# Kernel tuning notes

Measured on AMD Instinct MI355X. Metric: run time of the kernel, lower is better.

Reference implementation:

```python
import jax, jax.numpy as jnp
import numpy as np

DIM = 384
NUM_HEADS = 12
HEAD_DIM = DIM // NUM_HEADS  # 32
SCALE = HEAD_DIM ** -0.5
B, N = 4, 2048


def setup_inputs() -> dict:
    key = jax.random.key(0)
    k0, k1, k2, k3 = jax.random.split(key, 4)
    x = jax.random.normal(k0, (B, N, DIM), dtype=jnp.float32)
    # nn.Linear(dim, 3*dim, bias=False): y = x @ W_qkv, W_qkv is [C, 3C]
    W_qkv = jax.random.normal(k1, (DIM, 3 * DIM), dtype=jnp.float32) * (DIM ** -0.5)
    # nn.Linear(dim, dim): y = x @ W_proj + b_proj, W_proj is [C, C]
    W_proj = jax.random.normal(k2, (DIM, DIM), dtype=jnp.float32) * (DIM ** -0.5)
    b_proj = jax.random.normal(k3, (DIM,), dtype=jnp.float32) * 0.01
    return {"x": x, "W_qkv": W_qkv, "W_proj": W_proj, "b_proj": b_proj}


def reference(x, W_qkv, W_proj, b_proj):
    b, n, c = x.shape
    qkv = (x @ W_qkv).reshape(b, n, 3, NUM_HEADS, HEAD_DIM)
    qkv = jnp.transpose(qkv, (2, 0, 3, 1, 4))  # [3, B, H, N, hd]
    q, k, v = qkv[0], qkv[1], qkv[2]
    # full attention: softmax(q k^T * scale) v
    attn = jnp.einsum('bhqd,bhkd->bhqk', q, k) * SCALE  # [B,H,N,N]
    attn = jax.nn.softmax(attn, axis=-1)
    out = jnp.einsum('bhqk,bhkd->bhqd', attn, v)  # [B,H,N,hd]
    out = jnp.transpose(out, (0, 2, 1, 3)).reshape(b, n, c)
    return out @ W_proj + b_proj
```

## Files before the change

kernel.cpp:

```cpp
#include <hip/hip_runtime.h>

constexpr int BB  = 4;
constexpr int SEQ = 2048;
constexpr int CC  = 384;
constexpr int C3  = 1152;
constexpr int NH  = 12;
constexpr int HD  = 32;
constexpr float SCALE = 0.17677669529663689f;
constexpr float LOG2E = 1.4426950408889634f;
constexpr float KSC   = SCALE * LOG2E;
constexpr size_t KV_BYTES = (size_t)2 * BB * NH * SEQ * HD * 2;
constexpr size_t WT_BYTES = ((size_t)C3 * CC + (size_t)CC * CC) * 2;
constexpr size_t XB_BYTES = (size_t)BB * SEQ * CC * 2;

typedef __attribute__((ext_vector_type(8))) short short8_t;
typedef __attribute__((ext_vector_type(4))) float floatx4;

#if __has_builtin(__builtin_amdgcn_exp2f)
#define EXP2F __builtin_amdgcn_exp2f
#else
#define EXP2F __builtin_exp2f
#endif

__device__ __forceinline__ unsigned short f2bf(float f) {
    unsigned int u = __builtin_bit_cast(unsigned int, f);
    u += 0x7fffu + ((u >> 16) & 1u);
    return (unsigned short)(u >> 16);
}
__device__ __forceinline__ unsigned int pk_rn(float lo, float hi) {
    return __builtin_amdgcn_perm(__builtin_bit_cast(unsigned int, hi) + 0x8000u,
                                 __builtin_bit_cast(unsigned int, lo) + 0x8000u,
                                 0x07060302u);
}
__device__ __forceinline__ unsigned int cvtpk(float lo, float hi) {
    unsigned int r;
    asm("v_cvt_pk_bf16_f32 %0, %1, %2" : "=v"(r) : "v"(lo), "v"(hi));
    return r;
}
__device__ __forceinline__ short8_t pack8(float4 a, float4 b) {
    uint4 u;
    u.x = pk_rn(a.x, a.y); u.y = pk_rn(a.z, a.w);
    u.z = pk_rn(b.x, b.y); u.w = pk_rn(b.z, b.w);
    return __builtin_bit_cast(short8_t, u);
}

__device__ __forceinline__ void vstore(unsigned short* vb, short8_t a, short8_t b) {
    const uint4 ua = __builtin_bit_cast(uint4, a);
    const uint4 ub = __builtin_bit_cast(uint4, b);
    *(uint2*)(vb)      = (uint2){ua.x, ua.y};
    *(uint2*)(vb + 8)  = (uint2){ua.z, ua.w};
    *(uint2*)(vb + 16) = (uint2){ub.x, ub.y};
    *(uint2*)(vb + 24) = (uint2){ub.z, ub.w};
}

__global__ __launch_bounds__(256) void prep_kernel(
    const float* __restrict__ x, const float* __restrict__ wqkv,
    const float* __restrict__ wproj,
    unsigned short* __restrict__ wqkvT, unsigned short* __restrict__ wprojT,
    unsigned short* __restrict__ xb)
{
    const int bid = blockIdx.x;
    if (bid >= 144) {
        const size_t base = (size_t)(bid - 144) * 2048 + threadIdx.x * 8;
        const float4 a = *(const float4*)(x + base);
        const float4 b = *(const float4*)(x + base + 4);
        uint4 u;
        u.x = pk_rn(a.x, a.y); u.y = pk_rn(a.z, a.w);
        u.z = pk_rn(b.x, b.y); u.w = pk_rn(b.z, b.w);
        *(uint4*)(xb + base) = u;
        return;
    }
    __shared__ float ls[64][68];
    const float* src; unsigned short* dst; int SN, k0, n0;
    if (bid < 108) {
        src = wqkv; dst = wqkvT; SN = C3;
        k0 = (bid / 18) * 64; n0 = (bid % 18) * 64;
    } else {
        const int b2 = bid - 108;
        src = wproj; dst = wprojT; SN = CC;
        k0 = (b2 / 6) * 64; n0 = (b2 % 6) * 64;
    }
    const int t  = threadIdx.x;
    const int rr = t >> 4, cc4 = (t & 15) * 4;
#pragma unroll
    for (int p = 0; p < 4; ++p) {
        const int row = p * 16 + rr;
        const float4 v = *(const float4*)&src[(size_t)(k0 + row) * SN + n0 + cc4];
        ls[row][cc4] = v.x; ls[row][cc4 + 1] = v.y;
        ls[row][cc4 + 2] = v.z; ls[row][cc4 + 3] = v.w;
    }
    __syncthreads();
#pragma unroll
    for (int p = 0; p < 4; ++p) {
        const int nrow = p * 16 + rr;
        uint2 u;
        u.x = pk_rn(ls[cc4][nrow],     ls[cc4 + 1][nrow]);
        u.y = pk_rn(ls[cc4 + 2][nrow], ls[cc4 + 3][nrow]);
        *(uint2*)&dst[(size_t)(n0 + nrow) * CC + k0 + cc4] = u;
    }
}

__global__ __launch_bounds__(256) void qkv_fast(
    const unsigned short* __restrict__ xb,
    const unsigned short* __restrict__ wT,
    unsigned short* __restrict__ qb,
    unsigned short* __restrict__ kv)
{
    __shared__ __align__(16) unsigned short As[2][128][40];
    __shared__ __align__(16) unsigned short Bs[2][128][40];

    const int mt   = blockIdx.x & 63;
    const int nb   = blockIdx.x >> 6;
    const int tid  = threadIdx.x;
    const int wid  = tid >> 6;
    const int lane = tid & 63;
    const int quad = lane >> 4;
    const int col  = lane & 15;
    const int wr   = wid >> 1, wc = wid & 1;
    const int m0 = mt * 128, n0 = nb * 128;

    const int arow = tid >> 1;
    const int aoff = (tid & 1) * 16;

    floatx4 acc[4][4];
#pragma unroll
    for (int i = 0; i < 4; ++i)
#pragma unroll
        for (int j = 0; j < 4; ++j) acc[i][j] = (floatx4){0.f, 0.f, 0.f, 0.f};

    const unsigned short* xrow = xb + (size_t)(m0 + arow) * CC + aoff;
    const unsigned short* wrow = wT + (size_t)(n0 + arow) * CC + aoff;

    short8_t ast0, ast1, bst0, bst1;
    ast0 = *(const short8_t*)xrow;
    ast1 = *(const short8_t*)(xrow + 8);
    bst0 = *(const short8_t*)wrow;
    bst1 = *(const short8_t*)(wrow + 8);
    *(short8_t*)&As[0][arow][aoff]     = ast0;
    *(short8_t*)&As[0][arow][aoff + 8] = ast1;
    *(short8_t*)&Bs[0][arow][aoff]     = bst0;
    *(short8_t*)&Bs[0][arow][aoff + 8] = bst1;

    for (int it = 0; it < CC / 32; ++it) {
        const int kn = (it + 1 < CC / 32) ? (it + 1) * 32 : 0;
        ast0 = *(const short8_t*)(xrow + kn);
        ast1 = *(const short8_t*)(xrow + kn + 8);
        bst0 = *(const short8_t*)(wrow + kn);
        bst1 = *(const short8_t*)(wrow + kn + 8);

        __syncthreads();
        const int p = it & 1;
        short8_t af[4], bf[4];
#pragma unroll
        for (int i = 0; i < 4; ++i)
            af[i] = *(const short8_t*)&As[p][wr * 64 + i * 16 + col][quad * 8];
#pragma unroll
        for (int j = 0; j < 4; ++j)
            bf[j] = *(const short8_t*)&Bs[p][wc * 64 + j * 16 + col][quad * 8];
#pragma unroll
        for (int j = 0; j < 4; ++j)
#pragma unroll
            for (int i = 0; i < 4; ++i)
                acc[i][j] = __builtin_amdgcn_mfma_f32_16x16x32_bf16(af[i], bf[j], acc[i][j], 0, 0, 0);

        *(short8_t*)&As[p ^ 1][arow][aoff]     = ast0;
        *(short8_t*)&As[p ^ 1][arow][aoff + 8] = ast1;
        *(short8_t*)&Bs[p ^ 1][arow][aoff]     = bst0;
        *(short8_t*)&Bs[p ^ 1][arow][aoff + 8] = bst1;
    }

    const int t = nb / 3;
#pragma unroll
    for (int i = 0; i < 4; ++i) {
        const int mg = m0 + wr * 64 + i * 16 + quad * 4;
        if (t == 0) {
#pragma unroll
            for (int j = 0; j < 4; ++j) {
                const int n = n0 + wc * 64 + j * 16 + col;
#pragma unroll
                for (int r = 0; r < 4; ++r)
                    qb[(size_t)(mg + r) * CC + n] = f2bf(acc[i][j][r]);
            }
        } else if (t == 1) {
            const int b = mg >> 11, s = mg & (SEQ - 1);
#pragma unroll
            for (int j = 0; j < 4; ++j) {
                const int rem = n0 - CC + wc * 64 + j * 16 + col;
                const int h = rem >> 5, d = rem & 31;
                unsigned short* kp = kv + ((size_t)(b * NH + h) * SEQ + s) * HD + d;
#pragma unroll
                for (int r = 0; r < 4; ++r)
                    kp[(size_t)r * HD] = f2bf(acc[i][j][r] * KSC);
            }
        } else {
            const int b = mg >> 11, s = mg & (SEQ - 1);
            unsigned short* vtb = kv + (size_t)BB * NH * SEQ * HD;
#pragma unroll
            for (int j = 0; j < 4; ++j) {
                const int rem = n0 - 2 * CC + wc * 64 + j * 16 + col;
                const int h = rem >> 5, d = rem & 31;
                uint2 u;
                u.x = pk_rn(acc[i][j][0], acc[i][j][1]);
                u.y = pk_rn(acc[i][j][2], acc[i][j][3]);
                *(uint2*)&vtb[((size_t)(b * NH + h) * HD + d) * SEQ + s] = u;
            }
        }
    }
}

__global__ __launch_bounds__(256, 3) void attn_kernel(
    const unsigned short* __restrict__ kv,
    const unsigned short* __restrict__ qb,
    unsigned short* __restrict__ ab)
{
    const int bid  = blockIdx.x;
    const int qp   = bid / 48;
    const int bh   = bid % 48;
    const int h    = bh % NH;
    const int b    = bh / NH;
    const int w    = threadIdx.x >> 6;
    const int lane = threadIdx.x & 63;
    const int quad = lane >> 4;
    const int col  = lane & 15;
    const int tid  = threadIdx.x;

    const unsigned short* K  = kv + (size_t)bh * SEQ * HD;
    const unsigned short* VT = kv + (size_t)BB * NH * SEQ * HD + (size_t)bh * HD * SEQ;

    __shared__ __align__(16) unsigned short Vt[2][32][136];

    const int drow_s = tid >> 3, voff_s = (tid & 7) * 16;
    const int vbase  = ((tid & 6) >> 1) * 32 + (tid & 1) * 4;

    const unsigned short* Kf = K + (size_t)col * HD + quad * 8;

    int qrow[2];
    short8_t qf[2];
#pragma unroll
    for (int t = 0; t < 2; ++t) {
        qrow[t] = b * SEQ + qp * 128 + (w + 4 * t) * 16 + col;
        qf[t] = *(const short8_t*)(qb + (size_t)qrow[t] * CC + h * HD + quad * 8);
    }

    short8_t ones;
#pragma unroll
    for (int e = 0; e < 8; ++e) ones[e] = (short)0x3F80;

    floatx4 o[2][2];
    floatx4 lacc[2];
#pragma unroll
    for (int t = 0; t < 2; ++t) {
        lacc[t] = (floatx4){0.f, 0.f, 0.f, 0.f};
#pragma unroll
        for (int i = 0; i < 2; ++i) o[t][i] = (floatx4){0.f, 0.f, 0.f, 0.f};
    }
    const float ci = -10.f * LOG2E;
    const floatx4 cinit = {ci, ci, ci, ci};

    short8_t v0a = *(const short8_t*)(VT + (size_t)drow_s * SEQ + voff_s);
    short8_t v0b = *(const short8_t*)(VT + (size_t)drow_s * SEQ + voff_s + 8);
    vstore(&Vt[0][drow_s][vbase], v0a, v0b);

    short8_t kaf[4][2];
#pragma unroll
    for (int c = 0; c < 4; ++c) {
        kaf[c][0] = *(const short8_t*)(Kf + (size_t)(c * 32) * HD);
        kaf[c][1] = *(const short8_t*)(Kf + (size_t)(c * 32 + 16) * HD);
    }

    for (int it = 0; it < SEQ / 128; ++it) {
        const int kn = ((it + 1) * 128) & (SEQ - 1);
        v0a = *(const short8_t*)(VT + (size_t)drow_s * SEQ + kn + voff_s);
        v0b = *(const short8_t*)(VT + (size_t)drow_s * SEQ + kn + voff_s + 8);
        const unsigned short* Kn = Kf + (size_t)kn * HD;

        __syncthreads();
        const int p = it & 1;

        short8_t va[4][2];
#pragma unroll
        for (int c = 0; c < 4; ++c) {
            const int c32 = c * 32;
            va[c][0] = *(const short8_t*)&Vt[p][col][c32 + quad * 8];
            va[c][1] = *(const short8_t*)&Vt[p][16 + col][c32 + quad * 8];
        }

        floatx4 s0[2], s1[2];
        __builtin_amdgcn_s_setprio(1);
#pragma unroll
        for (int t = 0; t < 2; ++t) {
            s0[t] = __builtin_amdgcn_mfma_f32_16x16x32_bf16(kaf[0][0], qf[t], cinit, 0, 0, 0);
            s1[t] = __builtin_amdgcn_mfma_f32_16x16x32_bf16(kaf[0][1], qf[t], cinit, 0, 0, 0);
        }
        __builtin_amdgcn_s_setprio(0);
        kaf[0][0] = *(const short8_t*)(Kn);
        kaf[0][1] = *(const short8_t*)(Kn + (size_t)16 * HD);

#pragma unroll
        for (int c = 0; c < 4; ++c) {
            floatx4 n0[2], n1[2];
            if (c < 3) {
                __builtin_amdgcn_s_setprio(1);
#pragma unroll
                for (int t = 0; t < 2; ++t) {
                    n0[t] = __builtin_amdgcn_mfma_f32_16x16x32_bf16(kaf[c + 1][0], qf[t], cinit, 0, 0, 0);
                    n1[t] = __builtin_amdgcn_mfma_f32_16x16x32_bf16(kaf[c + 1][1], qf[t], cinit, 0, 0, 0);
                }
                __builtin_amdgcn_s_setprio(0);
                kaf[c + 1][0] = *(const short8_t*)(Kn + (size_t)((c + 1) * 32) * HD);
                kaf[c + 1][1] = *(const short8_t*)(Kn + (size_t)((c + 1) * 32 + 16) * HD);
            }

            short8_t pb[2];
#pragma unroll
            for (int t = 0; t < 2; ++t) {
                const float p00 = EXP2F(s0[t][0]), p01 = EXP2F(s0[t][1]);
                const float p02 = EXP2F(s0[t][2]), p03 = EXP2F(s0[t][3]);
                const float p10 = EXP2F(s1[t][0]), p11 = EXP2F(s1[t][1]);
                const float p12 = EXP2F(s1[t][2]), p13 = EXP2F(s1[t][3]);
                const uint4 pu = {cvtpk(p00, p01), cvtpk(p02, p03),
                                  cvtpk(p10, p11), cvtpk(p12, p13)};
                pb[t] = __builtin_bit_cast(short8_t, pu);
            }
            __builtin_amdgcn_s_setprio(1);
#pragma unroll
            for (int t = 0; t < 2; ++t) {
                o[t][0] = __builtin_amdgcn_mfma_f32_16x16x32_bf16(va[c][0], pb[t], o[t][0], 0, 0, 0);
                o[t][1] = __builtin_amdgcn_mfma_f32_16x16x32_bf16(va[c][1], pb[t], o[t][1], 0, 0, 0);
                lacc[t] = __builtin_amdgcn_mfma_f32_16x16x32_bf16(ones, pb[t], lacc[t], 0, 0, 0);
            }
            __builtin_amdgcn_s_setprio(0);
            if (c < 3) {
#pragma unroll
                for (int t = 0; t < 2; ++t) { s0[t] = n0[t]; s1[t] = n1[t]; }
            }
        }

        vstore(&Vt[p ^ 1][drow_s][vbase], v0a, v0b);
    }

#pragma unroll
    for (int t = 0; t < 2; ++t) {
        const float inv = 1.f / lacc[t][0];
        unsigned short* op = ab + (size_t)qrow[t] * CC + h * HD;
#pragma unroll
        for (int i = 0; i < 2; ++i) {
            uint2 u;
            u.x = pk_rn(o[t][i][0] * inv, o[t][i][1] * inv);
            u.y = pk_rn(o[t][i][2] * inv, o[t][i][3] * inv);
            *(uint2*)&op[i * 16 + quad * 4] = u;
        }
    }
}

__global__ __launch_bounds__(512) void proj_fast(
    const unsigned short* __restrict__ ab,
    const unsigned short* __restrict__ wT,
    const float* __restrict__ bias,
    float* __restrict__ out)
{
    __shared__ __align__(16) unsigned short Bs[2][384][32];

    const int mt   = blockIdx.x;
    const int tid  = threadIdx.x;
    const int wid  = tid >> 6;
    const int wn   = wid & 3;
    const int wm   = wid >> 2;
    const int lane = tid & 63;
    const int quad = lane >> 4;
    const int col  = lane & 15;
    const int m0   = mt * 32;

    floatx4 acc[6];
#pragma unroll
    for (int j = 0; j < 6; ++j) acc[j] = (floatx4){0.f, 0.f, 0.f, 0.f};

    const unsigned short* arow = ab + (size_t)(m0 + wm * 16 + col) * CC + quad * 8;

    const int f1 = tid;
    const int f2 = 512 + tid;
    const bool has2 = tid < 256;
    const unsigned short* wp1 = wT + (size_t)(f1 >> 1) * CC + (f1 & 1) * 16;
    const unsigned short* wp2 = wT + (size_t)(f2 >> 1) * CC + (f2 & 1) * 16;

    short8_t bA0, bA1, bB0, bB1;
    short8_t af;
    {
        bA0 = *(const short8_t*)wp1;
        bA1 = *(const short8_t*)(wp1 + 8);
        if (has2) {
            bB0 = *(const short8_t*)wp2;
            bB1 = *(const short8_t*)(wp2 + 8);
        }
        af = *(const short8_t*)arow;
        *(short8_t*)&Bs[0][f1 >> 1][(f1 & 1) * 16]     = bA0;
        *(short8_t*)&Bs[0][f1 >> 1][(f1 & 1) * 16 + 8] = bA1;
        if (has2) {
            *(short8_t*)&Bs[0][f2 >> 1][(f2 & 1) * 16]     = bB0;
            *(short8_t*)&Bs[0][f2 >> 1][(f2 & 1) * 16 + 8] = bB1;
        }
    }

    for (int it = 0; it < CC / 32; ++it) {
        const int kn = (it + 1 < CC / 32) ? (it + 1) * 32 : 0;
        bA0 = *(const short8_t*)(wp1 + kn);
        bA1 = *(const short8_t*)(wp1 + kn + 8);
        if (has2) {
            bB0 = *(const short8_t*)(wp2 + kn);
            bB1 = *(const short8_t*)(wp2 + kn + 8);
        }
        const short8_t afn = *(const short8_t*)(arow + kn);

        __syncthreads();
        const int p = it & 1;
        short8_t bf[6];
#pragma unroll
        for (int j = 0; j < 6; ++j)
            bf[j] = *(const short8_t*)&Bs[p][wn * 96 + j * 16 + col][quad * 8];
#pragma unroll
        for (int j = 0; j < 6; ++j)
            acc[j] = __builtin_amdgcn_mfma_f32_16x16x32_bf16(af, bf[j], acc[j], 0, 0, 0);

        *(short8_t*)&Bs[p ^ 1][f1 >> 1][(f1 & 1) * 16]     = bA0;
        *(short8_t*)&Bs[p ^ 1][f1 >> 1][(f1 & 1) * 16 + 8] = bA1;
        if (has2) {
            *(short8_t*)&Bs[p ^ 1][f2 >> 1][(f2 & 1) * 16]     = bB0;
            *(short8_t*)&Bs[p ^ 1][f2 >> 1][(f2 & 1) * 16 + 8] = bB1;
        }
        af = afn;
    }

#pragma unroll
    for (int j = 0; j < 6; ++j) {
        const int n = wn * 96 + j * 16 + col;
        const float bv = bias[n];
#pragma unroll
        for (int r = 0; r < 4; ++r)
            out[(size_t)(m0 + wm * 16 + quad * 4 + r) * CC + n] = acc[j][r] + bv;
    }
}

__global__ __launch_bounds__(256) void qkv_lds(
    const float* __restrict__ x, const float* __restrict__ w,
    float* __restrict__ dq, unsigned short* __restrict__ kv)
{
    __shared__ __align__(16) unsigned short wt[128 * 40];
    const int mt = blockIdx.x & 63, nb = blockIdx.x >> 6;
    const int tid = threadIdx.x, wid = tid >> 6, lane = tid & 63;
    const int quad = lane >> 4, col = lane & 15;
    const int wr = wid >> 1, wc = wid & 1;
    const int m0 = mt * 128, n0 = nb * 128;
    const int sn = tid >> 1, skg = (tid & 1) * 4;

    floatx4 acc[4][4];
#pragma unroll
    for (int i = 0; i < 4; ++i)
#pragma unroll
        for (int j = 0; j < 4; ++j) acc[i][j] = (floatx4){0.f, 0.f, 0.f, 0.f};
    const float* xbase = x + (size_t)(m0 + wr * 64 + col) * CC;

    for (int kb = 0; kb < CC; kb += 32) {
        float wv[4][4];
#pragma unroll
        for (int s = 0; s < 4; ++s) {
            const int k = kb + (skg + s) * 4;
#pragma unroll
            for (int j = 0; j < 4; ++j) wv[s][j] = w[(size_t)(k + j) * C3 + n0 + sn];
        }
        short8_t af[4];
#pragma unroll
        for (int i = 0; i < 4; ++i) {
            const float* xr = xbase + (size_t)i * 16 * CC + kb + quad * 8;
            af[i] = pack8(*(const float4*)xr, *(const float4*)(xr + 4));
        }
        __syncthreads();
#pragma unroll
        for (int s = 0; s < 4; ++s) {
            ushort4 u;
            u.x = f2bf(wv[s][0]); u.y = f2bf(wv[s][1]);
            u.z = f2bf(wv[s][2]); u.w = f2bf(wv[s][3]);
            *(ushort4*)&wt[sn * 40 + (skg + s) * 4] = u;
        }
        __syncthreads();
#pragma unroll
        for (int j = 0; j < 4; ++j) {
            const short8_t bf = *(const short8_t*)&wt[(wc * 64 + j * 16 + col) * 40 + quad * 8];
#pragma unroll
            for (int i = 0; i < 4; ++i)
                acc[i][j] = __builtin_amdgcn_mfma_f32_16x16x32_bf16(af[i], bf, acc[i][j], 0, 0, 0);
        }
    }
    const int t = nb / 3;
#pragma unroll
    for (int i = 0; i < 4; ++i) {
        const int mg = m0 + wr * 64 + i * 16 + quad * 4;
        if (t == 0) {
#pragma unroll
            for (int j = 0; j < 4; ++j) {
                const int n = n0 + wc * 64 + j * 16 + col;
#pragma unroll
                for (int r = 0; r < 4; ++r) dq[(size_t)(mg + r) * CC + n] = acc[i][j][r];
            }
        } else if (t == 1) {
            const int b = mg >> 11, s = mg & (SEQ - 1);
#pragma unroll
            for (int j = 0; j < 4; ++j) {
                const int rem = n0 - CC + wc * 64 + j * 16 + col;
                const int h = rem >> 5, d = rem & 31;
                unsigned short* kp = kv + ((size_t)(b * NH + h) * SEQ + s) * HD + d;
#pragma unroll
                for (int r = 0; r < 4; ++r) kp[(size_t)r * HD] = f2bf(acc[i][j][r]);
            }
        } else {
            const int b = mg >> 11, s = mg & (SEQ - 1);
            unsigned short* vtb = kv + (size_t)BB * NH * SEQ * HD;
#pragma unroll
            for (int j = 0; j < 4; ++j) {
                const int rem = n0 - 2 * CC + wc * 64 + j * 16 + col;
                const int h = rem >> 5, d = rem & 31;
                uint2 u;
                u.x = pk_rn(acc[i][j][0], acc[i][j][1]);
                u.y = pk_rn(acc[i][j][2], acc[i][j][3]);
                *(uint2*)&vtb[((size_t)(b * NH + h) * HD + d) * SEQ + s] = u;
            }
        }
    }
}

__global__ __launch_bounds__(256) void attn_f32(
    const unsigned short* __restrict__ kv,
    float* qatt)
{
    const int bid  = blockIdx.x;
    const int qp   = bid / 48;
    const int bh   = bid % 48;
    const int h    = bh % NH;
    const int b    = bh / NH;
    const int w    = threadIdx.x >> 6;
    const int lane = threadIdx.x & 63;
    const int quad = lane >> 4;
    const int col  = lane & 15;
    const int tid  = threadIdx.x;

    const unsigned short* K  = kv + (size_t)bh * SEQ * HD;
    const unsigned short* VT = kv + (size_t)BB * NH * SEQ * HD + (size_t)bh * HD * SEQ;

    __shared__ __align__(16) unsigned short Kt[2][128][40];
    __shared__ __align__(16) unsigned short Vt[2][32][136];

    const int krow_s = tid >> 1, koff_s = (tid & 1) * 16;
    const int drow_s = tid >> 3, voff_s = (tid & 7) * 16;

    int qrow[2];
    short8_t qf[2];
    const float sc = SCALE * LOG2E;
#pragma unroll
    for (int t = 0; t < 2; ++t) {
        qrow[t] = b * SEQ + qp * 128 + (w + 4 * t) * 16 + col;
        const float* qpt = qatt + (size_t)qrow[t] * CC + h * HD + quad * 8;
        const float4 a0 = *(const float4*)qpt;
        const float4 a1 = *(const float4*)(qpt + 4);
        const float4 s0 = {a0.x * sc, a0.y * sc, a0.z * sc, a0.w * sc};
        const float4 s1 = {a1.x * sc, a1.y * sc, a1.z * sc, a1.w * sc};
        qf[t] = pack8(s0, s1);
    }

    short8_t ones;
#pragma unroll
    for (int e = 0; e < 8; ++e) ones[e] = (short)0x3F80;

    floatx4 o[2][2];
    floatx4 lacc[2];
#pragma unroll
    for (int t = 0; t < 2; ++t) {
        lacc[t] = (floatx4){0.f, 0.f, 0.f, 0.f};
#pragma unroll
        for (int i = 0; i < 2; ++i) o[t][i] = (floatx4){0.f, 0.f, 0.f, 0.f};
    }
    const float ci = -10.f * LOG2E;
    const floatx4 cinit = {ci, ci, ci, ci};

    short8_t k0a = *(const short8_t*)(K + (size_t)krow_s * HD + koff_s);
    short8_t k0b = *(const short8_t*)(K + (size_t)krow_s * HD + koff_s + 8);
    short8_t v0a = *(const short8_t*)(VT + (size_t)drow_s * SEQ + voff_s);
    short8_t v0b = *(const short8_t*)(VT + (size_t)drow_s * SEQ + voff_s + 8);
    *(short8_t*)&Kt[0][krow_s][koff_s]     = k0a;
    *(short8_t*)&Kt[0][krow_s][koff_s + 8] = k0b;
    *(short8_t*)&Vt[0][drow_s][voff_s]     = v0a;
    *(short8_t*)&Vt[0][drow_s][voff_s + 8] = v0b;

    for (int it = 0; it < SEQ / 128; ++it) {
        const int kn = ((it + 1) * 128) & (SEQ - 1);
        k0a = *(const short8_t*)(K + (size_t)(kn + krow_s) * HD + koff_s);
        k0b = *(const short8_t*)(K + (size_t)(kn + krow_s) * HD + koff_s + 8);
        v0a = *(const short8_t*)(VT + (size_t)drow_s * SEQ + kn + voff_s);
        v0b = *(const short8_t*)(VT + (size_t)drow_s * SEQ + kn + voff_s + 8);

        __syncthreads();
        const int p = it & 1;

#pragma unroll
        for (int c = 0; c < 4; ++c) {
            const int c32 = c * 32;
            const short8_t ka0 = *(const short8_t*)&Kt[p][c32 + col][quad * 8];
            const short8_t ka1 = *(const short8_t*)&Kt[p][c32 + 16 + col][quad * 8];
            const uint2 w0a = *(const uint2*)&Vt[p][col][c32 + quad * 4];
            const uint2 w0b = *(const uint2*)&Vt[p][col][c32 + 16 + quad * 4];
            const uint2 w1a = *(const uint2*)&Vt[p][16 + col][c32 + quad * 4];
            const uint2 w1b = *(const uint2*)&Vt[p][16 + col][c32 + 16 + quad * 4];
            const short8_t va0 = __builtin_bit_cast(short8_t, (uint4){w0a.x, w0a.y, w0b.x, w0b.y});
            const short8_t va1 = __builtin_bit_cast(short8_t, (uint4){w1a.x, w1a.y, w1b.x, w1b.y});
#pragma unroll
            for (int t = 0; t < 2; ++t) {
                const floatx4 s0 = __builtin_amdgcn_mfma_f32_16x16x32_bf16(ka0, qf[t], cinit, 0, 0, 0);
                const floatx4 s1 = __builtin_amdgcn_mfma_f32_16x16x32_bf16(ka1, qf[t], cinit, 0, 0, 0);
                const float p00 = EXP2F(s0[0]), p01 = EXP2F(s0[1]);
                const float p02 = EXP2F(s0[2]), p03 = EXP2F(s0[3]);
                const float p10 = EXP2F(s1[0]), p11 = EXP2F(s1[1]);
                const float p12 = EXP2F(s1[2]), p13 = EXP2F(s1[3]);
                const uint4 pu = {pk_rn(p00, p01), pk_rn(p02, p03),
                                  pk_rn(p10, p11), pk_rn(p12, p13)};
                const short8_t pb = __builtin_bit_cast(short8_t, pu);
                o[t][0] = __builtin_amdgcn_mfma_f32_16x16x32_bf16(va0, pb, o[t][0], 0, 0, 0);
                o[t][1] = __builtin_amdgcn_mfma_f32_16x16x32_bf16(va1, pb, o[t][1], 0, 0, 0);
                lacc[t] = __builtin_amdgcn_mfma_f32_16x16x32_bf16(ones, pb, lacc[t], 0, 0, 0);
            }
        }

        *(short8_t*)&Kt[p ^ 1][krow_s][koff_s]     = k0a;
        *(short8_t*)&Kt[p ^ 1][krow_s][koff_s + 8] = k0b;
        *(short8_t*)&Vt[p ^ 1][drow_s][voff_s]     = v0a;
        *(short8_t*)&Vt[p ^ 1][drow_s][voff_s + 8] = v0b;
    }

#pragma unroll
    for (int t = 0; t < 2; ++t) {
        const float inv = 1.f / lacc[t][0];
        float* op = qatt + (size_t)qrow[t] * CC + h * HD;
#pragma unroll
        for (int r = 0; r < 4; ++r) {
            op[quad * 4 + r]      = o[t][0][r] * inv;
            op[16 + quad * 4 + r] = o[t][1][r] * inv;
        }
    }
}

__global__ __launch_bounds__(256) void proj_lds(
    float* att, const float* __restrict__ wp, const float* __restrict__ bias)
{
    __shared__ __align__(16) unsigned short wt[CC * 40];
    const int mt = blockIdx.x, tid = threadIdx.x, wid = tid >> 6, lane = tid & 63;
    const int quad = lane >> 4, col = lane & 15;
    const int m0 = mt * 16;
    floatx4 acc[6];
#pragma unroll
    for (int j = 0; j < 6; ++j) acc[j] = (floatx4){0.f, 0.f, 0.f, 0.f};
    for (int kb = 0; kb < CC; kb += 32) {
        float gv[12][4];
#pragma unroll
        for (int g = 0; g < 12; ++g) {
            const int flat = tid + g * 256, n = flat % 384, kg = flat / 384;
#pragma unroll
            for (int j = 0; j < 4; ++j) gv[g][j] = wp[(size_t)(kb + kg * 4 + j) * CC + n];
        }
        __syncthreads();
#pragma unroll
        for (int g = 0; g < 12; ++g) {
            const int flat = tid + g * 256, n = flat % 384, kg = flat / 384;
            ushort4 u;
            u.x = f2bf(gv[g][0]); u.y = f2bf(gv[g][1]);
            u.z = f2bf(gv[g][2]); u.w = f2bf(gv[g][3]);
            *(ushort4*)&wt[n * 40 + kg * 4] = u;
        }
        __syncthreads();
        const float* ap = att + (size_t)(m0 + col) * CC + kb + quad * 8;
        const short8_t af = pack8(*(const float4*)ap, *(const float4*)(ap + 4));
#pragma unroll
        for (int j = 0; j < 6; ++j) {
            const short8_t pb = *(const short8_t*)&wt[(wid * 96 + j * 16 + col) * 40 + quad * 8];
            acc[j] = __builtin_amdgcn_mfma_f32_16x16x32_bf16(af, pb, acc[j], 0, 0, 0);
        }
    }
    __syncthreads();
#pragma unroll
    for (int j = 0; j < 6; ++j) {
        const int n = wid * 96 + j * 16 + col;
        const float bv = bias[n];
#pragma unroll
        for (int r = 0; r < 4; ++r)
            att[(size_t)(m0 + quad * 4 + r) * CC + n] = acc[j][r] + bv;
    }
}

__global__ void marker_kernel(float* out, float val, int nelem) {
    int i = blockIdx.x * 256 + threadIdx.x;
    if (i < nelem) out[i] = val;
}

extern "C" void kernel_launch(void* const* d_in, const int* in_sizes, int n_in,
                              void* d_out, int out_size, void* d_ws, size_t ws_size,
                              hipStream_t stream)
{
    const float* x     = (const float*)d_in[0];
    const float* wqkv  = (const float*)d_in[1];
    const float* wproj = (const float*)d_in[2];
    const float* bproj = (const float*)d_in[3];
    float* out = (float*)d_out;
    unsigned short* kv = (unsigned short*)d_ws;

    if (ws_size < KV_BYTES) {
        const float marker = 100.f + (float)(ws_size >> 20);
        marker_kernel<<<(out_size + 255) / 256, 256, 0, stream>>>(out, marker, out_size);
        return;
    }

    unsigned short* wqkvT  = kv + (size_t)2 * BB * NH * SEQ * HD;
    unsigned short* wprojT = wqkvT + (size_t)C3 * CC;
    unsigned short* xb     = wprojT + (size_t)CC * CC;

    if (ws_size >= KV_BYTES + WT_BYTES + XB_BYTES) {
        unsigned short* qb = (unsigned short*)d_out;
        prep_kernel<<<144 + 1536, 256, 0, stream>>>(x, wqkv, wproj, wqkvT, wprojT, xb);
        qkv_fast<<<576, 256, 0, stream>>>(xb, wqkvT, qb, kv);
        attn_kernel<<<16 * BB * NH, 256, 0, stream>>>(kv, qb, xb );
        proj_fast<<<BB * SEQ / 32, 512, 0, stream>>>(xb, wprojT, bproj, out);
    } else {
        qkv_lds<<<576, 256, 0, stream>>>(x, wqkv, out, kv);
        attn_f32<<<16 * BB * NH, 256, 0, stream>>>(kv, out);
        proj_lds<<<BB * SEQ / 16, 256, 0, stream>>>(out, wproj, bproj);
    }
}
```

Baseline: 132.9 us.

## Split attention over two key halves with a separate combine kernel

Splits each attention block's key range into two halves, doubling the grid from 768 to 1536 blocks so the GPU is better filled. Each half writes unnormalized fp32 partial outputs and row sums to workspace, and a new combine kernel adds them, normalizes and writes bf16. Occupancy is raised to 4 blocks per CU, and the QK software pipelining that precomputed the next chunk's scores is dropped. In exchange it adds an extra kernel launch, fp32 partial-buffer traffic, and a larger workspace requirement that could send execution down the slow fallback path.

```diff
diff --git a/kernel.cpp b/kernel.cpp
--- a/kernel.cpp
+++ b/kernel.cpp
@@ -12,6 +12,7 @@
 constexpr size_t KV_BYTES = (size_t)2 * BB * NH * SEQ * HD * 2;
 constexpr size_t WT_BYTES = ((size_t)C3 * CC + (size_t)CC * CC) * 2;
 constexpr size_t XB_BYTES = (size_t)BB * SEQ * CC * 2;
+constexpr size_t PART_BYTES = ((size_t)2 * BB * SEQ * NH * HD + (size_t)2 * BB * SEQ * NH) * 4;
 
 typedef __attribute__((ext_vector_type(8))) short short8_t;
 typedef __attribute__((ext_vector_type(4))) float floatx4;
@@ -208,14 +209,17 @@
     }
 }
 
-__global__ __launch_bounds__(256, 3) void attn_kernel(
+__global__ __launch_bounds__(256, 4) void attn_kernel(
     const unsigned short* __restrict__ kv,
     const unsigned short* __restrict__ qb,
-    unsigned short* __restrict__ ab)
+    float* __restrict__ opart,
+    float* __restrict__ lpart)
 {
     const int bid  = blockIdx.x;
-    const int qp   = bid / 48;
-    const int bh   = bid % 48;
+    const int half = bid / 768;
+    const int rem  = bid % 768;
+    const int qp   = rem / 48;
+    const int bh   = rem % 48;
     const int h    = bh % NH;
     const int b    = bh / NH;
     const int w    = threadIdx.x >> 6;
@@ -224,8 +228,9 @@
     const int col  = lane & 15;
     const int tid  = threadIdx.x;
 
-    const unsigned short* K  = kv + (size_t)bh * SEQ * HD;
-    const unsigned short* VT = kv + (size_t)BB * NH * SEQ * HD + (size_t)bh * HD * SEQ;
+    const unsigned short* K  = kv + (size_t)bh * SEQ * HD + (size_t)half * 1024 * HD;
+    const unsigned short* VT = kv + (size_t)BB * NH * SEQ * HD + (size_t)bh * HD * SEQ
+                                  + (size_t)half * 1024;
 
     __shared__ __align__(16) unsigned short Vt[2][32][136];
 
@@ -268,8 +273,8 @@
         kaf[c][1] = *(const short8_t*)(Kf + (size_t)(c * 32 + 16) * HD);
     }
 
-    for (int it = 0; it < SEQ / 128; ++it) {
-        const int kn = ((it + 1) * 128) & (SEQ - 1);
+    for (int it = 0; it < 1024 / 128; ++it) {
+        const int kn = ((it + 1) * 128) & 1023;
         v0a = *(const short8_t*)(VT + (size_t)drow_s * SEQ + kn + voff_s);
         v0b = *(const short8_t*)(VT + (size_t)drow_s * SEQ + kn + voff_s + 8);
         const unsigned short* Kn = Kf + (size_t)kn * HD;
@@ -285,31 +290,18 @@
             va[c][1] = *(const short8_t*)&Vt[p][16 + col][c32 + quad * 8];
         }
 
-        floatx4 s0[2], s1[2];
-        __builtin_amdgcn_s_setprio(1);
-#pragma unroll
-        for (int t = 0; t < 2; ++t) {
-            s0[t] = __builtin_amdgcn_mfma_f32_16x16x32_bf16(kaf[0][0], qf[t], cinit, 0, 0, 0);
-            s1[t] = __builtin_amdgcn_mfma_f32_16x16x32_bf16(kaf[0][1], qf[t], cinit, 0, 0, 0);
-        }
-        __builtin_amdgcn_s_setprio(0);
-        kaf[0][0] = *(const short8_t*)(Kn);
-        kaf[0][1] = *(const short8_t*)(Kn + (size_t)16 * HD);
-
 #pragma unroll
         for (int c = 0; c < 4; ++c) {
-            floatx4 n0[2], n1[2];
-            if (c < 3) {
-                __builtin_amdgcn_s_setprio(1);
-#pragma unroll
-                for (int t = 0; t < 2; ++t) {
-                    n0[t] = __builtin_amdgcn_mfma_f32_16x16x32_bf16(kaf[c + 1][0], qf[t], cinit, 0, 0, 0);
-                    n1[t] = __builtin_amdgcn_mfma_f32_16x16x32_bf16(kaf[c + 1][1], qf[t], cinit, 0, 0, 0);
-                }
-                __builtin_amdgcn_s_setprio(0);
-                kaf[c + 1][0] = *(const short8_t*)(Kn + (size_t)((c + 1) * 32) * HD);
-                kaf[c + 1][1] = *(const short8_t*)(Kn + (size_t)((c + 1) * 32 + 16) * HD);
-            }
+            floatx4 s0[2], s1[2];
+            __builtin_amdgcn_s_setprio(1);
+#pragma unroll
+            for (int t = 0; t < 2; ++t) {
+                s0[t] = __builtin_amdgcn_mfma_f32_16x16x32_bf16(kaf[c][0], qf[t], cinit, 0, 0, 0);
+                s1[t] = __builtin_amdgcn_mfma_f32_16x16x32_bf16(kaf[c][1], qf[t], cinit, 0, 0, 0);
+            }
+            __builtin_amdgcn_s_setprio(0);
+            kaf[c][0] = *(const short8_t*)(Kn + (size_t)(c * 32) * HD);
+            kaf[c][1] = *(const short8_t*)(Kn + (size_t)(c * 32 + 16) * HD);
 
             short8_t pb[2];
 #pragma unroll
@@ -330,27 +322,41 @@
                 lacc[t] = __builtin_amdgcn_mfma_f32_16x16x32_bf16(ones, pb[t], lacc[t], 0, 0, 0);
             }
             __builtin_amdgcn_s_setprio(0);
-            if (c < 3) {
-#pragma unroll
-                for (int t = 0; t < 2; ++t) { s0[t] = n0[t]; s1[t] = n1[t]; }
-            }
         }
 
         vstore(&Vt[p ^ 1][drow_s][vbase], v0a, v0b);
     }
 
+    const size_t hofs = (size_t)half * BB * SEQ * NH;
 #pragma unroll
     for (int t = 0; t < 2; ++t) {
-        const float inv = 1.f / lacc[t][0];
-        unsigned short* op = ab + (size_t)qrow[t] * CC + h * HD;
+        const size_t rh = hofs + (size_t)qrow[t] * NH + h;
+        if (quad == 0) lpart[rh] = lacc[t][0];
+        float* op = opart + rh * HD;
 #pragma unroll
         for (int i = 0; i < 2; ++i) {
-            uint2 u;
-            u.x = pk_rn(o[t][i][0] * inv, o[t][i][1] * inv);
-            u.y = pk_rn(o[t][i][2] * inv, o[t][i][3] * inv);
-            *(uint2*)&op[i * 16 + quad * 4] = u;
-        }
-    }
+            const float4 v = {o[t][i][0], o[t][i][1], o[t][i][2], o[t][i][3]};
+            *(float4*)&op[i * 16 + quad * 4] = v;
+        }
+    }
+}
+
+__global__ __launch_bounds__(256) void combine_kernel(
+    const float* __restrict__ opart, const float* __restrict__ lpart,
+    unsigned short* __restrict__ ab)
+{
+    const size_t idx = (size_t)blockIdx.x * 256 + threadIdx.x;
+    const int d4 = (int)(idx & 7) * 4;
+    const size_t rh = idx >> 3;
+    const size_t half1 = (size_t)BB * SEQ * NH;
+    const float inv = 1.f / (lpart[rh] + lpart[half1 + rh]);
+    const float4 a = *(const float4*)&opart[rh * HD + d4];
+    const float4 c = *(const float4*)&opart[(half1 + rh) * HD + d4];
+    const int row = (int)(rh / NH), h = (int)(rh % NH);
+    uint2 u;
+    u.x = pk_rn((a.x + c.x) * inv, (a.y + c.y) * inv);
+    u.y = pk_rn((a.z + c.z) * inv, (a.w + c.w) * inv);
+    *(uint2*)&ab[(size_t)row * CC + h * HD + d4] = u;
 }
 
 __global__ __launch_bounds__(512) void proj_fast(
@@ -717,12 +723,15 @@
     unsigned short* wqkvT  = kv + (size_t)2 * BB * NH * SEQ * HD;
     unsigned short* wprojT = wqkvT + (size_t)C3 * CC;
     unsigned short* xb     = wprojT + (size_t)CC * CC;
-
-    if (ws_size >= KV_BYTES + WT_BYTES + XB_BYTES) {
+    float* opart = (float*)(xb + (size_t)BB * SEQ * CC);
+    float* lpart = opart + (size_t)2 * BB * SEQ * NH * HD;
+
+    if (ws_size >= KV_BYTES + WT_BYTES + XB_BYTES + PART_BYTES) {
         unsigned short* qb = (unsigned short*)d_out;
         prep_kernel<<<144 + 1536, 256, 0, stream>>>(x, wqkv, wproj, wqkvT, wprojT, xb);
         qkv_fast<<<576, 256, 0, stream>>>(xb, wqkvT, qb, kv);
-        attn_kernel<<<16 * BB * NH, 256, 0, stream>>>(kv, qb, xb );
+        attn_kernel<<<2 * 16 * BB * NH, 256, 0, stream>>>(kv, qb, opart, lpart);
+        combine_kernel<<<BB * SEQ * NH * 8 / 256, 256, 0, stream>>>(opart, lpart, xb);
         proj_fast<<<BB * SEQ / 32, 512, 0, stream>>>(xb, wprojT, bproj, out);
     } else {
         qkv_lds<<<576, 256, 0, stream>>>(x, wqkv, out, kv);
```

Result: slower. 178.1 us (+34.0%).
